# Performance work log

Measured on AMD Instinct MI355X. Metric: run time of the kernel, lower is better.

## Reference

```python
import jax, jax.numpy as jnp
import numpy as np

BATCH = 8192
NUM_CLASSES = 10000
FEAT_DIM = 256


def setup_inputs() -> dict:
    key = jax.random.key(0)
    k1, k2, k3 = jax.random.split(key, 3)
    x = jax.random.normal(k1, (BATCH, FEAT_DIM), dtype=jnp.float32)
    labels = jax.random.randint(k2, (BATCH,), 0, NUM_CLASSES, dtype=jnp.int64)
    centers = jax.random.normal(k3, (NUM_CLASSES, FEAT_DIM), dtype=jnp.float32)
    return {"x": x, "labels": labels, "centers": centers}


def reference(x, labels, centers):
    batch_size = x.shape[0]
    num_classes = centers.shape[0]
    # distmat[b,c] = ||x_b||^2 + ||center_c||^2 - 2 <x_b, center_c>   [B, C]
    x_sq = jnp.sum(x * x, axis=1, keepdims=True)            # [B, 1]
    c_sq = jnp.sum(centers * centers, axis=1)[None, :]      # [1, C]
    distmat = x_sq + c_sq - 2.0 * jnp.einsum('bd,cd->bc', x, centers)
    # mask: one-hot of labels over classes
    mask = (labels[:, None] == jnp.arange(num_classes)[None, :]).astype(distmat.dtype)
    dist = distmat * mask
    # torch clamps ALL entries (masked zeros become 1e-12) before summing
    loss = jnp.sum(jnp.clip(dist, 1e-12, 1e12)) / batch_size
    return loss
```

## Files before the change

kernel.cpp:

```cpp
#include <hip/hip_runtime.h>


#define TPB1 512
#define TPB2 1024

__global__ __launch_bounds__(TPB1) void centerloss_partial(
    const float* __restrict__ x,
    const int* __restrict__ labels,
    const float* __restrict__ centers,
    float* __restrict__ partial,
    int B)
{
    const int lane = threadIdx.x & 63;
    const int b    = (blockIdx.x * TPB1 + threadIdx.x) >> 6;
    if (b >= B) return;

    const int lbl = labels[b];
    const float4 xv = ((const float4*)(x       + (size_t)b   * 256))[lane];
    const float4 cv = ((const float4*)(centers + (size_t)lbl * 256))[lane];

    float v = xv.x * xv.x + xv.y * xv.y + xv.z * xv.z + xv.w * xv.w;
    v += cv.x * cv.x + cv.y * cv.y + cv.z * cv.z + cv.w * cv.w;
    v -= 2.0f * (xv.x * cv.x + xv.y * cv.y + xv.z * cv.z + xv.w * cv.w);

    #pragma unroll
    for (int off = 32; off > 0; off >>= 1)
        v += __shfl_down(v, off, 64);

    if (lane == 0)
        partial[b] = fminf(fmaxf(v, 1e-12f), 1e12f);
}

__global__ __launch_bounds__(TPB2) void centerloss_final(
    const float* __restrict__ partial,
    float* __restrict__ out,
    int n, int B, int C)
{
    float v = 0.0f;
    for (int i = threadIdx.x; i < n; i += TPB2)
        v += partial[i];

    #pragma unroll
    for (int off = 32; off > 0; off >>= 1)
        v += __shfl_down(v, off, 64);

    __shared__ float s[TPB2 / 64];
    if ((threadIdx.x & 63) == 0) s[threadIdx.x >> 6] = v;
    __syncthreads();
    if (threadIdx.x == 0) {
        float t = 0.0f;
        #pragma unroll
        for (int i = 0; i < TPB2 / 64; ++i) t += s[i];
        double loss = (double)t / (double)B + (double)(C - 1) * 1e-12;
        out[0] = (float)loss;
    }
}

extern "C" void kernel_launch(void* const* d_in, const int* in_sizes, int n_in,
                              void* d_out, int out_size, void* d_ws, size_t ws_size,
                              hipStream_t stream)
{
    const float* x       = (const float*)d_in[0];
    const int*   labels  = (const int*)d_in[1];
    const float* centers = (const float*)d_in[2];

    const int B = in_sizes[1];
    const int D = in_sizes[0] / B;
    const int C = in_sizes[2] / D;

    float* partial = (float*)d_ws;
    float* out     = (float*)d_out;

    const int nblocks = (B * 64 + TPB1 - 1) / TPB1;
    centerloss_partial<<<nblocks, TPB1, 0, stream>>>(x, labels, centers, partial, B);
    centerloss_final<<<1, TPB2, 0, stream>>>(partial, out, B, B, C);
}
```

Measured before the change: 69.47 us.

## Fuse partial and final reduction into one kernel with atomic accumulation

Merges the per-sample distance kernel and the single-block final reduction into one kernel. Each block reduces its waves through shared memory and atomically adds a scaled partial into the output, which is zeroed beforehand with a memset. This removes the second kernel launch and the partial buffer round trip. In exchange it adds a memset, 1024 float atomics on one address, and a summation order that is no longer deterministic.

Measured after the change: 79.56 us. +14.5%, slower.

```diff
diff --git a/kernel.cpp b/kernel.cpp
--- a/kernel.cpp
+++ b/kernel.cpp
@@ -1,58 +1,48 @@
 #include <hip/hip_runtime.h>
 
 
-#define TPB1 512
-#define TPB2 1024
+#define TPB 512
+#define WPB (TPB / 64)
 
-__global__ __launch_bounds__(TPB1) void centerloss_partial(
+__global__ __launch_bounds__(TPB) void centerloss_fused(
     const float* __restrict__ x,
     const int* __restrict__ labels,
     const float* __restrict__ centers,
-    float* __restrict__ partial,
-    int B)
+    float* __restrict__ out,
+    int B, int C, float invB)
 {
     const int lane = threadIdx.x & 63;
-    const int b    = (blockIdx.x * TPB1 + threadIdx.x) >> 6;
-    if (b >= B) return;
+    const int wid  = threadIdx.x >> 6;
+    const int b    = (int)((blockIdx.x * TPB + threadIdx.x) >> 6);
 
-    const int lbl = labels[b];
-    const float4 xv = ((const float4*)(x       + (size_t)b   * 256))[lane];
-    const float4 cv = ((const float4*)(centers + (size_t)lbl * 256))[lane];
+    float v = 0.0f;
+    const bool valid = (b < B);
+    if (valid) {
+        const int lbl = labels[b];
+        const float4 xv = ((const float4*)(x       + (size_t)b   * 256))[lane];
+        const float4 cv = ((const float4*)(centers + (size_t)lbl * 256))[lane];
 
-    float v = xv.x * xv.x + xv.y * xv.y + xv.z * xv.z + xv.w * xv.w;
-    v += cv.x * cv.x + cv.y * cv.y + cv.z * cv.z + cv.w * cv.w;
-    v -= 2.0f * (xv.x * cv.x + xv.y * cv.y + xv.z * cv.z + xv.w * cv.w);
+        v  = xv.x * xv.x + xv.y * xv.y + xv.z * xv.z + xv.w * xv.w;
+        v += cv.x * cv.x + cv.y * cv.y + cv.z * cv.z + cv.w * cv.w;
+        v -= 2.0f * (xv.x * cv.x + xv.y * cv.y + xv.z * cv.z + xv.w * cv.w);
+    }
 
     #pragma unroll
     for (int off = 32; off > 0; off >>= 1)
         v += __shfl_down(v, off, 64);
 
+    __shared__ float s[WPB];
     if (lane == 0)
-        partial[b] = fminf(fmaxf(v, 1e-12f), 1e12f);
-}
+        s[wid] = valid ? fminf(fmaxf(v, 1e-12f), 1e12f) * invB : 0.0f;
+    __syncthreads();
 
-__global__ __launch_bounds__(TPB2) void centerloss_final(
-    const float* __restrict__ partial,
-    float* __restrict__ out,
-    int n, int B, int C)
-{
-    float v = 0.0f;
-    for (int i = threadIdx.x; i < n; i += TPB2)
-        v += partial[i];
-
-    #pragma unroll
-    for (int off = 32; off > 0; off >>= 1)
-        v += __shfl_down(v, off, 64);
-
-    __shared__ float s[TPB2 / 64];
-    if ((threadIdx.x & 63) == 0) s[threadIdx.x >> 6] = v;
-    __syncthreads();
     if (threadIdx.x == 0) {
         float t = 0.0f;
         #pragma unroll
-        for (int i = 0; i < TPB2 / 64; ++i) t += s[i];
-        double loss = (double)t / (double)B + (double)(C - 1) * 1e-12;
-        out[0] = (float)loss;
+        for (int i = 0; i < WPB; ++i) t += s[i];
+        if (blockIdx.x == 0)
+            t += (float)((double)(C - 1) * 1e-12);
+        atomicAdd(out, t);
     }
 }
 
@@ -68,10 +58,13 @@
     const int D = in_sizes[0] / B;
     const int C = in_sizes[2] / D;
 
-    float* partial = (float*)d_ws;
-    float* out     = (float*)d_out;
+    float* out = (float*)d_out;
 
-    const int nblocks = (B * 64 + TPB1 - 1) / TPB1;
-    centerloss_partial<<<nblocks, TPB1, 0, stream>>>(x, labels, centers, partial, B);
-    centerloss_final<<<1, TPB2, 0, stream>>>(partial, out, B, B, C);
+    (void)d_ws; (void)ws_size;
+
+    hipMemsetAsync(out, 0, sizeof(float), stream);
+
+    const int nblocks = (B * 64 + TPB - 1) / TPB;
+    centerloss_fused<<<nblocks, TPB, 0, stream>>>(x, labels, centers, out,
+                                                  B, C, 1.0f / (float)B);
 }
```
